# Performance work log

Hardware: AMD Instinct MI355X
Metric: run time of the kernel (lower is better)

## Reference

```python
import jax, jax.numpy as jnp
import numpy as np

D_MODEL = 512
N_HEADS = 8
HEAD_DIM = 64
INNER = N_HEADS * HEAD_DIM
PAD = 128  # flash-attention style tile padding used by the custom kernel


def setup_inputs() -> dict:
    key = jax.random.key(0)
    ks = jax.random.split(key, 5)
    B, S = 2, 2048
    scale = 0.02
    return {
        "hidden_states": jax.random.normal(ks[0], (B, S, D_MODEL), dtype=jnp.float32),
        "Wq": jax.random.normal(ks[1], (D_MODEL, INNER), dtype=jnp.float32) * scale,
        "Wk": jax.random.normal(ks[2], (D_MODEL, INNER), dtype=jnp.float32) * scale,
        "Wv": jax.random.normal(ks[3], (D_MODEL, INNER), dtype=jnp.float32) * scale,
        "Wo": jax.random.normal(ks[4], (INNER, D_MODEL), dtype=jnp.float32) * scale,
    }


def _padded_attention(q, k, v):
    """Emulates torch.ops.knl.fwd: pad seq to a multiple of PAD, run
    non-causal scaled dot-product attention masking padded keys, then
    slice back to the original length. q,k,v: [B, S, INNER]."""
    B, S, _ = q.shape
    pad_len = (-S) % PAD
    Sp = S + pad_len
    pad_cfg = ((0, 0), (0, pad_len), (0, 0))
    qp = jnp.pad(q, pad_cfg)
    kp = jnp.pad(k, pad_cfg)
    vp = jnp.pad(v, pad_cfg)
    # [B, H, Sp, hd]
    qh = qp.reshape(B, Sp, N_HEADS, HEAD_DIM).transpose(0, 2, 1, 3)
    kh = kp.reshape(B, Sp, N_HEADS, HEAD_DIM).transpose(0, 2, 1, 3)
    vh = vp.reshape(B, Sp, N_HEADS, HEAD_DIM).transpose(0, 2, 1, 3)
    scale = 1.0 / np.sqrt(HEAD_DIM).astype(np.float32)
    scores = jnp.einsum("bhqd,bhkd->bhqk", qh, kh) * scale  # [B,H,Sp,Sp]
    key_valid = jnp.arange(Sp) < S  # mask out padded keys
    scores = jnp.where(key_valid[None, None, None, :], scores, jnp.float32(-1e30))
    probs = jax.nn.softmax(scores, axis=-1)
    out = jnp.einsum("bhqk,bhkd->bhqd", probs, vh)  # [B,H,Sp,hd]
    out = out.transpose(0, 2, 1, 3).reshape(B, Sp, INNER)
    return out[:, :S, :]


def reference(hidden_states, Wq, Wk, Wv, Wo):
    q = hidden_states @ Wq
    k = hidden_states @ Wk
    v = hidden_states @ Wv
    attn = _padded_attention(q, k, v)
    return attn @ Wo
```

## Files before the change

### kernel.cpp

```cpp
#include <hip/hip_runtime.h>

using bf16 = __bf16;
using bf16x4 = __attribute__((ext_vector_type(4))) __bf16;
using bf16x8 = __attribute__((ext_vector_type(8))) __bf16;
using floatx4 = __attribute__((ext_vector_type(4))) float;
using half4 = __attribute__((ext_vector_type(4))) _Float16;
using half8 = __attribute__((ext_vector_type(8))) _Float16;

#define D_MODEL 512
#define S_LEN 2048
#define HD 64
#define NH 8
#define M_TOT 4096
#define RS 72
#define NSPLIT 4
#define KSPAN (S_LEN / NSPLIT)
#define QSCALE 0.18033688f

__device__ __forceinline__ bf16x8 ld8(const bf16* p) {
    return *reinterpret_cast<const bf16x8*>(p);
}
__device__ __forceinline__ void gl_lds16(const bf16* g, bf16* l) {
    __builtin_amdgcn_global_load_lds(
        (const __attribute__((address_space(1))) void*)g,
        (__attribute__((address_space(3))) void*)l, 16, 0, 0);
}

__global__ __launch_bounds__(256) void prep(const float* __restrict__ w0,
                                            const float* __restrict__ w1,
                                            const float* __restrict__ w2,
                                            const float* __restrict__ w3,
                                            const float* __restrict__ X,
                                            bf16* __restrict__ WT,
                                            bf16* __restrict__ Xb) {
    int z = blockIdx.z;
    if (z == 4) {
        int i = (blockIdx.x * 256 + threadIdx.x) * 8;
        float4 a = *reinterpret_cast<const float4*>(X + i);
        float4 b = *reinterpret_cast<const float4*>(X + i + 4);
        bf16x8 o;
        o[0] = (bf16)a.x; o[1] = (bf16)a.y; o[2] = (bf16)a.z; o[3] = (bf16)a.w;
        o[4] = (bf16)b.x; o[5] = (bf16)b.y; o[6] = (bf16)b.z; o[7] = (bf16)b.w;
        *reinterpret_cast<bf16x8*>(Xb + i) = o;
        return;
    }
    if (blockIdx.x >= 256) return;
    __shared__ float t[32][33];
    const float* in = z == 0 ? w0 : z == 1 ? w1 : z == 2 ? w2 : w3;
    bf16* o = WT + (size_t)z * D_MODEL * D_MODEL;
    int x = threadIdx.x & 31;
    int y = threadIdx.x >> 5;
    int k0 = (blockIdx.x & 15) * 32, n0 = (blockIdx.x >> 4) * 32;
    for (int r = y; r < 32; r += 8) t[r][x] = in[(size_t)(k0 + r) * D_MODEL + n0 + x];
    __syncthreads();
    for (int r = y; r < 32; r += 8) o[(size_t)(n0 + r) * D_MODEL + k0 + x] = (bf16)t[x][r];
}

__global__ __launch_bounds__(256) void transpose_v(const bf16* __restrict__ v,
                                                   bf16* __restrict__ vt) {
    __shared__ bf16 t[32][34];
    int bh = blockIdx.z;
    int s0 = blockIdx.x * 32, d0 = blockIdx.y * 32;
    const bf16* in = v + (size_t)bh * S_LEN * HD;
    bf16* o = vt + (size_t)bh * HD * S_LEN;
    int x = threadIdx.x & 31;
    int y = threadIdx.x >> 5;
    for (int r = y; r < 32; r += 8) t[r][x] = in[(size_t)(s0 + r) * HD + d0 + x];
    __syncthreads();
    for (int r = y; r < 32; r += 8) o[(size_t)(d0 + r) * S_LEN + s0 + x] = t[x][r];
}

__global__ __launch_bounds__(256) void gemm_qkv(const bf16* __restrict__ X,
                                                const bf16* __restrict__ WT3,
                                                bf16* __restrict__ qkv) {
    __shared__ __align__(16) bf16 As[64 * 64];
    __shared__ __align__(16) bf16 Bs[64 * 64];
    int lane = threadIdx.x & 63, wave = threadIdx.x >> 6;
    int l15 = lane & 15, quad = lane >> 4;
    const bf16* wt = WT3 + (size_t)blockIdx.z * D_MODEL * D_MODEL;
    bf16* dst = qkv + (size_t)blockIdx.z * M_TOT * D_MODEL;
    int m0 = blockIdx.x * 64;
    int n0 = blockIdx.y * 64;
    int wm = (wave & 1) * 32, wn = (wave >> 1) * 32;
    float oscale = (blockIdx.z == 0) ? QSCALE : 1.0f;

    int sr = lane >> 3;
    int sc = (lane & 7) ^ sr;
    const bf16* gA = X  + (size_t)(m0 + wave * 16 + sr) * D_MODEL + sc * 8;
    const bf16* gB = wt + (size_t)(n0 + wave * 16 + sr) * D_MODEL + sc * 8;
    bf16* ldsA = &As[(wave * 16) * 64];
    bf16* ldsB = &Bs[(wave * 16) * 64];
    int rx = l15 & 7;

    floatx4 acc[2][2] = {};
    for (int k0 = 0; k0 < D_MODEL; k0 += 64) {
        __syncthreads();
        gl_lds16(gA + k0, ldsA);
        gl_lds16(gA + (size_t)8 * D_MODEL + k0, ldsA + 8 * 64);
        gl_lds16(gB + k0, ldsB);
        gl_lds16(gB + (size_t)8 * D_MODEL + k0, ldsB + 8 * 64);
        __syncthreads();
        bf16x8 af[2][2], bfr[2][2];
        #pragma unroll
        for (int mt = 0; mt < 2; mt++)
            #pragma unroll
            for (int kh = 0; kh < 2; kh++)
                af[mt][kh] = ld8(&As[(wm + mt * 16 + l15) * 64 + (((quad + 4 * kh) ^ rx)) * 8]);
        #pragma unroll
        for (int nt = 0; nt < 2; nt++)
            #pragma unroll
            for (int kh = 0; kh < 2; kh++)
                bfr[nt][kh] = ld8(&Bs[(wn + nt * 16 + l15) * 64 + (((quad + 4 * kh) ^ rx)) * 8]);
        #pragma unroll
        for (int mt = 0; mt < 2; mt++)
            #pragma unroll
            for (int nt = 0; nt < 2; nt++) {
                acc[mt][nt] = __builtin_amdgcn_mfma_f32_16x16x32_bf16(af[mt][0], bfr[nt][0], acc[mt][nt], 0, 0, 0);
                acc[mt][nt] = __builtin_amdgcn_mfma_f32_16x16x32_bf16(af[mt][1], bfr[nt][1], acc[mt][nt], 0, 0, 0);
            }
    }

    #pragma unroll
    for (int mt = 0; mt < 2; mt++)
        #pragma unroll
        for (int nt = 0; nt < 2; nt++)
            #pragma unroll
            for (int r = 0; r < 4; r++) {
                int m = m0 + wm + mt * 16 + quad * 4 + r;
                int n = n0 + wn + nt * 16 + l15;
                int b = m >> 11, s = m & 2047;
                int h = n >> 6,  d = n & 63;
                dst[((size_t)(b * NH + h) * S_LEN + s) * HD + d] = (bf16)(acc[mt][nt][r] * oscale);
            }
}

__global__ __launch_bounds__(256) void attn_split(const bf16* __restrict__ qg,
                                                  const bf16* __restrict__ kg,
                                                  const bf16* __restrict__ vt,
                                                  _Float16* __restrict__ Opart,
                                                  float* __restrict__ lsum) {
    __shared__ __align__(16) bf16 Kl[64 * RS];
    __shared__ __align__(16) bf16 Vl[64 * RS];
    __shared__ __align__(16) bf16 Pl[64 * RS];
    int tid = threadIdx.x;
    int lane = tid & 63, wave = tid >> 6;
    int l15 = lane & 15, quad = lane >> 4;
    int bh = blockIdx.y, split = blockIdx.z;
    int q0 = blockIdx.x * 64;
    const bf16* qb = qg + (size_t)bh * S_LEN * HD;
    const bf16* kb = kg + (size_t)bh * S_LEN * HD + (size_t)split * KSPAN * HD;
    const bf16* vb = vt + (size_t)bh * HD * S_LEN + split * KSPAN;
    int q = q0 + wave * 16 + l15;
    bf16x8 qf0 = ld8(qb + (size_t)q * HD + quad * 8);
    bf16x8 qf1 = ld8(qb + (size_t)q * HD + 32 + quad * 8);
    floatx4 O[4] = {};
    float l_i = 0.f;
    int rbase = tid >> 3;
    int c8 = (tid & 7) * 8;
    int dv = tid >> 2;
    int c16 = (tid & 3) * 16;

    for (int kt = 0; kt < KSPAN; kt += 64) {
        __syncthreads();
        #pragma unroll
        for (int rr = 0; rr < 64; rr += 32) {
            int r = rr + rbase;
            bf16x8 kk = ld8(kb + (size_t)(kt + r) * HD + c8);
            *reinterpret_cast<bf16x8*>(&Kl[r * RS + c8]) = kk;
        }
        {
            bf16x8 v0 = ld8(vb + (size_t)dv * S_LEN + kt + c16);
            bf16x8 v1 = ld8(vb + (size_t)dv * S_LEN + kt + c16 + 8);
            *reinterpret_cast<bf16x8*>(&Vl[dv * RS + c16]) = v0;
            *reinterpret_cast<bf16x8*>(&Vl[dv * RS + c16 + 8]) = v1;
        }
        __syncthreads();

        floatx4 sc[4];
        #pragma unroll
        for (int nt = 0; nt < 4; nt++) {
            floatx4 z = {};
            bf16x8 a0 = ld8(&Kl[(nt * 16 + l15) * RS + quad * 8]);
            bf16x8 a1 = ld8(&Kl[(nt * 16 + l15) * RS + 32 + quad * 8]);
            z = __builtin_amdgcn_mfma_f32_16x16x32_bf16(a0, qf0, z, 0, 0, 0);
            z = __builtin_amdgcn_mfma_f32_16x16x32_bf16(a1, qf1, z, 0, 0, 0);
            sc[nt] = z;
        }

        #pragma unroll
        for (int nt = 0; nt < 4; nt++) {
            bf16x4 pk;
            #pragma unroll
            for (int r = 0; r < 4; r++) {
                float p = exp2f(sc[nt][r]);
                l_i += p;
                pk[r] = (bf16)p;
            }
            *reinterpret_cast<bf16x4*>(&Pl[(wave * 16 + l15) * RS + nt * 16 + quad * 4]) = pk;
        }
        __syncthreads();

        bf16x8 pb0 = ld8(&Pl[(wave * 16 + l15) * RS + quad * 8]);
        bf16x8 pb1 = ld8(&Pl[(wave * 16 + l15) * RS + 32 + quad * 8]);
        #pragma unroll
        for (int nt = 0; nt < 4; nt++) {
            bf16x8 v0 = ld8(&Vl[(nt * 16 + l15) * RS + quad * 8]);
            bf16x8 v1 = ld8(&Vl[(nt * 16 + l15) * RS + 32 + quad * 8]);
            O[nt] = __builtin_amdgcn_mfma_f32_16x16x32_bf16(v0, pb0, O[nt], 0, 0, 0);
            O[nt] = __builtin_amdgcn_mfma_f32_16x16x32_bf16(v1, pb1, O[nt], 0, 0, 0);
        }
    }

    l_i += __shfl_xor(l_i, 16, 64);
    l_i += __shfl_xor(l_i, 32, 64);

    size_t obase = (((size_t)(split * 16 + bh)) * S_LEN + q) * HD;
    #pragma unroll
    for (int nt = 0; nt < 4; nt++) {
        half4 h;
        h[0] = (_Float16)O[nt][0]; h[1] = (_Float16)O[nt][1];
        h[2] = (_Float16)O[nt][2]; h[3] = (_Float16)O[nt][3];
        *reinterpret_cast<half4*>(&Opart[obase + nt * 16 + quad * 4]) = h;
    }
    if (quad == 0)
        lsum[((size_t)(split * 16 + bh)) * S_LEN + q] = l_i;
}

__global__ __launch_bounds__(256) void attn_merge(const _Float16* __restrict__ Opart,
                                                  const float* __restrict__ lsum,
                                                  bf16* __restrict__ ctx) {
    int idx = blockIdx.x * 256 + threadIdx.x;
    int g = idx & 7;
    int q = (idx >> 3) & 2047;
    int bh = idx >> 14;
    int b = bh >> 3, h = bh & 7;
    float l = 0.f;
    #pragma unroll
    for (int s = 0; s < NSPLIT; s++) l += lsum[((size_t)(s * 16 + bh)) * S_LEN + q];
    float inv = 1.f / l;
    float o[8] = {};
    #pragma unroll
    for (int s = 0; s < NSPLIT; s++) {
        half8 hp = *reinterpret_cast<const half8*>(
            &Opart[(((size_t)(s * 16 + bh)) * S_LEN + q) * HD + g * 8]);
        #pragma unroll
        for (int j = 0; j < 8; j++) o[j] += (float)hp[j];
    }
    bf16x8 ob;
    #pragma unroll
    for (int j = 0; j < 8; j++) ob[j] = (bf16)(o[j] * inv);
    *reinterpret_cast<bf16x8*>(&ctx[((size_t)(b * S_LEN + q)) * D_MODEL + h * HD + g * 8]) = ob;
}

__global__ __launch_bounds__(256) void gemm_out(const bf16* __restrict__ Xc,
                                                const bf16* __restrict__ WoT,
                                                float* __restrict__ out) {
    __shared__ __align__(16) bf16 As[64 * 64];
    __shared__ __align__(16) bf16 Bs[64 * 64];
    int lane = threadIdx.x & 63, wave = threadIdx.x >> 6;
    int l15 = lane & 15, quad = lane >> 4;
    int m0 = blockIdx.x * 64;
    int n0 = blockIdx.y * 64;
    int wm = (wave & 1) * 32, wn = (wave >> 1) * 32;

    int sr = lane >> 3;
    int sc = (lane & 7) ^ sr;
    const bf16* gA = Xc  + (size_t)(m0 + wave * 16 + sr) * D_MODEL + sc * 8;
    const bf16* gB = WoT + (size_t)(n0 + wave * 16 + sr) * D_MODEL + sc * 8;
    bf16* ldsA = &As[(wave * 16) * 64];
    bf16* ldsB = &Bs[(wave * 16) * 64];
    int rx = l15 & 7;

    floatx4 acc[2][2] = {};
    for (int k0 = 0; k0 < D_MODEL; k0 += 64) {
        __syncthreads();
        gl_lds16(gA + k0, ldsA);
        gl_lds16(gA + (size_t)8 * D_MODEL + k0, ldsA + 8 * 64);
        gl_lds16(gB + k0, ldsB);
        gl_lds16(gB + (size_t)8 * D_MODEL + k0, ldsB + 8 * 64);
        __syncthreads();
        bf16x8 af[2][2], bfr[2][2];
        #pragma unroll
        for (int mt = 0; mt < 2; mt++)
            #pragma unroll
            for (int kh = 0; kh < 2; kh++)
                af[mt][kh] = ld8(&As[(wm + mt * 16 + l15) * 64 + (((quad + 4 * kh) ^ rx)) * 8]);
        #pragma unroll
        for (int nt = 0; nt < 2; nt++)
            #pragma unroll
            for (int kh = 0; kh < 2; kh++)
                bfr[nt][kh] = ld8(&Bs[(wn + nt * 16 + l15) * 64 + (((quad + 4 * kh) ^ rx)) * 8]);
        #pragma unroll
        for (int mt = 0; mt < 2; mt++)
            #pragma unroll
            for (int nt = 0; nt < 2; nt++) {
                acc[mt][nt] = __builtin_amdgcn_mfma_f32_16x16x32_bf16(af[mt][0], bfr[nt][0], acc[mt][nt], 0, 0, 0);
                acc[mt][nt] = __builtin_amdgcn_mfma_f32_16x16x32_bf16(af[mt][1], bfr[nt][1], acc[mt][nt], 0, 0, 0);
            }
    }

    #pragma unroll
    for (int mt = 0; mt < 2; mt++)
        #pragma unroll
        for (int nt = 0; nt < 2; nt++)
            #pragma unroll
            for (int r = 0; r < 4; r++) {
                int m = m0 + wm + mt * 16 + quad * 4 + r;
                int n = n0 + wn + nt * 16 + l15;
                out[(size_t)m * D_MODEL + n] = acc[mt][nt][r];
            }
}

extern "C" void kernel_launch(void* const* d_in, const int* in_sizes, int n_in,
                              void* d_out, int out_size, void* d_ws, size_t ws_size,
                              hipStream_t stream) {
    const float* X  = (const float*)d_in[0];
    const float* Wq = (const float*)d_in[1];
    const float* Wk = (const float*)d_in[2];
    const float* Wv = (const float*)d_in[3];
    const float* Wo = (const float*)d_in[4];
    float* out = (float*)d_out;
    bf16* ws  = (bf16*)d_ws;

    bf16* Xb  = ws;
    bf16* WT  = Xb + (size_t)M_TOT * D_MODEL;
    bf16* qkv = WT + (size_t)4 * D_MODEL * D_MODEL;
    bf16* ctx = qkv + (size_t)3 * M_TOT * D_MODEL;
    _Float16* Opart = (_Float16*)(ctx + (size_t)M_TOT * D_MODEL);
    float* lbuf = (float*)(Opart + (size_t)NSPLIT * 16 * S_LEN * HD);
    bf16* VT = Xb;

    prep<<<dim3(1024, 1, 5), 256, 0, stream>>>(Wq, Wk, Wv, Wo, X, WT, Xb);
    gemm_qkv<<<dim3(64, 8, 3), 256, 0, stream>>>(Xb, WT, qkv);
    transpose_v<<<dim3(64, 2, 16), 256, 0, stream>>>(qkv + (size_t)2 * M_TOT * D_MODEL, VT);
    attn_split<<<dim3(32, 16, NSPLIT), 256, 0, stream>>>(qkv,
                                                         qkv + (size_t)M_TOT * D_MODEL,
                                                         VT, Opart, lbuf);
    attn_merge<<<dim3(16 * S_LEN * 8 / 256), 256, 0, stream>>>(Opart, lbuf, ctx);
    gemm_out<<<dim3(64, 8), 256, 0, stream>>>(ctx, WT + (size_t)3 * D_MODEL * D_MODEL, out);
}
```

Baseline: 132.5 us.

## Double query rows per wave and load K/V tiles via swizzled direct-to-LDS

```diff
diff --git a/kernel.cpp b/kernel.cpp
--- a/kernel.cpp
+++ b/kernel.cpp
@@ -139,91 +139,106 @@
                                                   const bf16* __restrict__ vt,
                                                   _Float16* __restrict__ Opart,
                                                   float* __restrict__ lsum) {
-    __shared__ __align__(16) bf16 Kl[64 * RS];
-    __shared__ __align__(16) bf16 Vl[64 * RS];
-    __shared__ __align__(16) bf16 Pl[64 * RS];
+    __shared__ __align__(16) bf16 Kl[64 * 64];
+    __shared__ __align__(16) bf16 Vl[64 * 64];
+    __shared__ __align__(16) bf16 Pl[128 * RS];
     int tid = threadIdx.x;
     int lane = tid & 63, wave = tid >> 6;
     int l15 = lane & 15, quad = lane >> 4;
     int bh = blockIdx.y, split = blockIdx.z;
-    int q0 = blockIdx.x * 64;
+    int q0 = blockIdx.x * 128;
     const bf16* qb = qg + (size_t)bh * S_LEN * HD;
     const bf16* kb = kg + (size_t)bh * S_LEN * HD + (size_t)split * KSPAN * HD;
     const bf16* vb = vt + (size_t)bh * HD * S_LEN + split * KSPAN;
-    int q = q0 + wave * 16 + l15;
-    bf16x8 qf0 = ld8(qb + (size_t)q * HD + quad * 8);
-    bf16x8 qf1 = ld8(qb + (size_t)q * HD + 32 + quad * 8);
-    floatx4 O[4] = {};
-    float l_i = 0.f;
-    int rbase = tid >> 3;
-    int c8 = (tid & 7) * 8;
-    int dv = tid >> 2;
-    int c16 = (tid & 3) * 16;
+
+    int qA = q0 + wave * 32 + l15;
+    int qB = qA + 16;
+    bf16x8 qf[2][2];
+    qf[0][0] = ld8(qb + (size_t)qA * HD + quad * 8);
+    qf[0][1] = ld8(qb + (size_t)qA * HD + 32 + quad * 8);
+    qf[1][0] = ld8(qb + (size_t)qB * HD + quad * 8);
+    qf[1][1] = ld8(qb + (size_t)qB * HD + 32 + quad * 8);
+    floatx4 O[2][4] = {};
+    float l_i[2] = {0.f, 0.f};
+
+    int sr = lane >> 3;
+    int sc = (lane & 7) ^ sr;
+    const bf16* gK = kb + (size_t)(wave * 16 + sr) * HD + sc * 8;
+    const bf16* gV = vb + (size_t)(wave * 16 + sr) * S_LEN + sc * 8;
+    bf16* ldsK = &Kl[(wave * 16) * 64];
+    bf16* ldsV = &Vl[(wave * 16) * 64];
+    int rx = l15 & 7;
 
     for (int kt = 0; kt < KSPAN; kt += 64) {
         __syncthreads();
-        #pragma unroll
-        for (int rr = 0; rr < 64; rr += 32) {
-            int r = rr + rbase;
-            bf16x8 kk = ld8(kb + (size_t)(kt + r) * HD + c8);
-            *reinterpret_cast<bf16x8*>(&Kl[r * RS + c8]) = kk;
+        gl_lds16(gK + (size_t)kt * HD, ldsK);
+        gl_lds16(gK + (size_t)(kt + 8) * HD, ldsK + 8 * 64);
+        gl_lds16(gV + kt, ldsV);
+        gl_lds16(gV + (size_t)8 * S_LEN + kt, ldsV + 8 * 64);
+        __syncthreads();
+
+        #pragma unroll
+        for (int qh = 0; qh < 2; qh++) {
+            floatx4 sc4[4];
+            #pragma unroll
+            for (int nt = 0; nt < 4; nt++) {
+                floatx4 z = {};
+                bf16x8 a0 = ld8(&Kl[(nt * 16 + l15) * 64 + (quad ^ rx) * 8]);
+                bf16x8 a1 = ld8(&Kl[(nt * 16 + l15) * 64 + ((quad + 4) ^ rx) * 8]);
+                z = __builtin_amdgcn_mfma_f32_16x16x32_bf16(a0, qf[qh][0], z, 0, 0, 0);
+                z = __builtin_amdgcn_mfma_f32_16x16x32_bf16(a1, qf[qh][1], z, 0, 0, 0);
+                sc4[nt] = z;
+            }
+            #pragma unroll
+            for (int nt = 0; nt < 4; nt++) {
+                bf16x4 pk;
+                #pragma unroll
+                for (int r = 0; r < 4; r++) {
+                    float p = exp2f(sc4[nt][r]);
+                    l_i[qh] += p;
+                    pk[r] = (bf16)p;
+                }
+                *reinterpret_cast<bf16x4*>(
+                    &Pl[(wave * 32 + qh * 16 + l15) * RS + nt * 16 + quad * 4]) = pk;
+            }
         }
-        {
-            bf16x8 v0 = ld8(vb + (size_t)dv * S_LEN + kt + c16);
-            bf16x8 v1 = ld8(vb + (size_t)dv * S_LEN + kt + c16 + 8);
-            *reinterpret_cast<bf16x8*>(&Vl[dv * RS + c16]) = v0;
-            *reinterpret_cast<bf16x8*>(&Vl[dv * RS + c16 + 8]) = v1;
+        __syncthreads();
+
+        bf16x8 pb[2][2];
+        #pragma unroll
+        for (int qh = 0; qh < 2; qh++) {
+            pb[qh][0] = ld8(&Pl[(wave * 32 + qh * 16 + l15) * RS + quad * 8]);
+            pb[qh][1] = ld8(&Pl[(wave * 32 + qh * 16 + l15) * RS + 32 + quad * 8]);
         }
-        __syncthreads();
-
-        floatx4 sc[4];
         #pragma unroll
         for (int nt = 0; nt < 4; nt++) {
-            floatx4 z = {};
-            bf16x8 a0 = ld8(&Kl[(nt * 16 + l15) * RS + quad * 8]);
-            bf16x8 a1 = ld8(&Kl[(nt * 16 + l15) * RS + 32 + quad * 8]);
-            z = __builtin_amdgcn_mfma_f32_16x16x32_bf16(a0, qf0, z, 0, 0, 0);
-            z = __builtin_amdgcn_mfma_f32_16x16x32_bf16(a1, qf1, z, 0, 0, 0);
-            sc[nt] = z;
+            bf16x8 v0 = ld8(&Vl[(nt * 16 + l15) * 64 + (quad ^ rx) * 8]);
+            bf16x8 v1 = ld8(&Vl[(nt * 16 + l15) * 64 + ((quad + 4) ^ rx) * 8]);
+            #pragma unroll
+            for (int qh = 0; qh < 2; qh++) {
+                O[qh][nt] = __builtin_amdgcn_mfma_f32_16x16x32_bf16(v0, pb[qh][0], O[qh][nt], 0, 0, 0);
+                O[qh][nt] = __builtin_amdgcn_mfma_f32_16x16x32_bf16(v1, pb[qh][1], O[qh][nt], 0, 0, 0);
+            }
         }
-
+    }
+
+    #pragma unroll
+    for (int qh = 0; qh < 2; qh++) {
+        float l = l_i[qh];
+        l += __shfl_xor(l, 16, 64);
+        l += __shfl_xor(l, 32, 64);
+        int q = (qh == 0) ? qA : qB;
+        size_t obase = (((size_t)(split * 16 + bh)) * S_LEN + q) * HD;
         #pragma unroll
         for (int nt = 0; nt < 4; nt++) {
-            bf16x4 pk;
-            #pragma unroll
-            for (int r = 0; r < 4; r++) {
-                float p = exp2f(sc[nt][r]);
-                l_i += p;
-                pk[r] = (bf16)p;
-            }
-            *reinterpret_cast<bf16x4*>(&Pl[(wave * 16 + l15) * RS + nt * 16 + quad * 4]) = pk;
+            half4 h;
+            h[0] = (_Float16)O[qh][nt][0]; h[1] = (_Float16)O[qh][nt][1];
+            h[2] = (_Float16)O[qh][nt][2]; h[3] = (_Float16)O[qh][nt][3];
+            *reinterpret_cast<half4*>(&Opart[obase + nt * 16 + quad * 4]) = h;
         }
-        __syncthreads();
-
-        bf16x8 pb0 = ld8(&Pl[(wave * 16 + l15) * RS + quad * 8]);
-        bf16x8 pb1 = ld8(&Pl[(wave * 16 + l15) * RS + 32 + quad * 8]);
-        #pragma unroll
-        for (int nt = 0; nt < 4; nt++) {
-            bf16x8 v0 = ld8(&Vl[(nt * 16 + l15) * RS + quad * 8]);
-            bf16x8 v1 = ld8(&Vl[(nt * 16 + l15) * RS + 32 + quad * 8]);
-            O[nt] = __builtin_amdgcn_mfma_f32_16x16x32_bf16(v0, pb0, O[nt], 0, 0, 0);
-            O[nt] = __builtin_amdgcn_mfma_f32_16x16x32_bf16(v1, pb1, O[nt], 0, 0, 0);
-        }
-    }
-
-    l_i += __shfl_xor(l_i, 16, 64);
-    l_i += __shfl_xor(l_i, 32, 64);
-
-    size_t obase = (((size_t)(split * 16 + bh)) * S_LEN + q) * HD;
-    #pragma unroll
-    for (int nt = 0; nt < 4; nt++) {
-        half4 h;
-        h[0] = (_Float16)O[nt][0]; h[1] = (_Float16)O[nt][1];
-        h[2] = (_Float16)O[nt][2]; h[3] = (_Float16)O[nt][3];
-        *reinterpret_cast<half4*>(&Opart[obase + nt * 16 + quad * 4]) = h;
-    }
-    if (quad == 0)
-        lsum[((size_t)(split * 16 + bh)) * S_LEN + q] = l_i;
+        if (quad == 0)
+            lsum[((size_t)(split * 16 + bh)) * S_LEN + q] = l;
+    }
 }
 
 __global__ __launch_bounds__(256) void attn_merge(const _Float16* __restrict__ Opart,
@@ -333,7 +348,7 @@
     prep<<<dim3(1024, 1, 5), 256, 0, stream>>>(Wq, Wk, Wv, Wo, X, WT, Xb);
     gemm_qkv<<<dim3(64, 8, 3), 256, 0, stream>>>(Xb, WT, qkv);
     transpose_v<<<dim3(64, 2, 16), 256, 0, stream>>>(qkv + (size_t)2 * M_TOT * D_MODEL, VT);
-    attn_split<<<dim3(32, 16, NSPLIT), 256, 0, stream>>>(qkv,
+    attn_split<<<dim3(16, 16, NSPLIT), 256, 0, stream>>>(qkv,
                                                          qkv + (size_t)M_TOT * D_MODEL,
                                                          VT, Opart, lbuf);
     attn_merge<<<dim3(16 * S_LEN * 8 / 256), 256, 0, stream>>>(Opart, lbuf, ctx);
```

New measurement: 131.3 us. Within noise of the previous version (-0.9%).
